# Kernel optimization log

Measured on AMD Instinct MI355X. Metric: run time of the kernel, lower is better.

Reference implementation:

```python
import jax, jax.numpy as jnp
import numpy as np

B, IMG_DIM, H, W = 2, 256, 64, 64
PC_C, PC_D = 16, 16          # voxel_dim = PC_C * PC_D = 256
VOXEL_DIM = PC_C * PC_D
QK_DIM = 256                 # out_channels of img_conv / voxel_conv


def _conv1x1(x, w, b):
    # x: [B, Cin, H, W], w: [Cout, Cin], b: [Cout]  (1x1 conv == per-pixel matmul)
    return jnp.einsum('bchw,oc->bohw', x, w) + b[None, :, None, None]


def setup_inputs() -> dict:
    key = jax.random.key(0)
    ks = jax.random.split(key, 10)
    s = 0.02
    return {
        'img': jax.random.normal(ks[0], (B, IMG_DIM, H, W), jnp.float32),
        'pc': jax.random.normal(ks[1], (B, PC_D, H, W, PC_C), jnp.float32),  # dense() layout [B,D,H,W,C]
        'img_conv_w': jax.random.normal(ks[2], (QK_DIM, IMG_DIM), jnp.float32) * s,
        'img_conv_b': jnp.zeros((QK_DIM,), jnp.float32),
        'voxel_conv_w': jax.random.normal(ks[3], (QK_DIM, VOXEL_DIM), jnp.float32) * s,
        'voxel_conv_b': jnp.zeros((QK_DIM,), jnp.float32),
        'img_v_w': jax.random.normal(ks[4], (IMG_DIM, IMG_DIM), jnp.float32) * s,
        'img_v_b': jnp.zeros((IMG_DIM,), jnp.float32),
        'voxel_v_w': jax.random.normal(ks[5], (VOXEL_DIM, VOXEL_DIM), jnp.float32) * s,
        'voxel_v_b': jnp.zeros((VOXEL_DIM,), jnp.float32),
    }


def reference(img, pc, img_conv_w, img_conv_b, voxel_conv_w, voxel_conv_b,
              img_v_w, img_v_b, voxel_v_w, voxel_v_b):
    b, c_img, h, w = img.shape
    # pc.dense() -> permute(0,4,1,2,3) -> [B, C, D, H, W] -> [B, C*D, H, W]
    pc = jnp.transpose(pc, (0, 4, 1, 2, 3))
    pcb, pcc, pcd, pch, pcw = pc.shape
    pc2 = pc.reshape(pcb, pcc * pcd, pch, pcw)
    n = h * w  # == pch * pcw (required by the bmms)

    img_q = _conv1x1(img, img_conv_w, img_conv_b).reshape(b, QK_DIM, n).transpose(0, 2, 1)  # [B, N, 256]
    pc_k = _conv1x1(pc2, voxel_conv_w, voxel_conv_b).reshape(b, QK_DIM, n)                  # [B, 256, N]
    # unscaled single-head cross attention, softmax over voxel positions
    attn = jax.nn.softmax(jnp.einsum('bnc,bcm->bnm', img_q, pc_k), axis=-1)                 # [B, N_img, N_pc]

    img_v = _conv1x1(img, img_v_w, img_v_b).reshape(b, c_img, n)                            # [B, C_img, N]
    img_v = jnp.einsum('bcn,bmn->bcm', img_v, attn).reshape(b, c_img, h, w)                 # img_v @ attn^T

    pc_v = _conv1x1(pc2, voxel_v_w, voxel_v_b).reshape(b, pcc * pcd, n)                     # [B, C*D, N]
    pc_v = jnp.einsum('bcn,bmn->bcm', pc_v, attn).reshape(b, pcc, pcd, pch, pcw)
    return (img_v, pc_v)
```

## Files before the change

### kernel.cpp

```cpp
#include <hip/hip_runtime.h>
#include <hip/hip_bf16.h>


typedef __hip_bfloat16 bf16;
typedef __attribute__((ext_vector_type(8))) short bf16x8;
typedef __attribute__((ext_vector_type(4))) float f32x4;

#define AS1 __attribute__((address_space(1)))
#define AS3 __attribute__((address_space(3)))

__device__ __forceinline__ void gld_lds16(const bf16* g, bf16* s) {
    __builtin_amdgcn_global_load_lds((const AS1 void*)g, (AS3 void*)s, 16, 0, 0);
}

__device__ __forceinline__ bf16x8 cvt8(const float* __restrict__ p) {
    const float4 a = *(const float4*)p;
    const float4 b = *(const float4*)(p + 4);
    bf16 t[8];
    t[0] = __float2bfloat16(a.x); t[1] = __float2bfloat16(a.y);
    t[2] = __float2bfloat16(a.z); t[3] = __float2bfloat16(a.w);
    t[4] = __float2bfloat16(b.x); t[5] = __float2bfloat16(b.y);
    t[6] = __float2bfloat16(b.z); t[7] = __float2bfloat16(b.w);
    return *(const bf16x8*)t;
}

__global__ __launch_bounds__(256) void proj_kernel(
    const float* __restrict__ img, const float* __restrict__ pc,
    const float* __restrict__ Wq,  const float* __restrict__ bq,
    const float* __restrict__ Wk,  const float* __restrict__ bk,
    const float* __restrict__ Wvi, const float* __restrict__ bvi,
    const float* __restrict__ Wvp, const float* __restrict__ bvp,
    bf16* __restrict__ Qw, bf16* __restrict__ Ktw, bf16* __restrict__ Vall)
{
    __shared__ __align__(16) bf16 XT[64][264];

    const int blk = blockIdx.x;
    const int s   = blk >> 8;
    const int b   = (blk >> 7) & 1;
    const int g   = (blk >> 6) & 1;
    const int n0  = (blk & 63) * 64;
    const int tid = threadIdx.x;

    if (s == 0) {
        const float* src = img + b * 1048576;
        for (int k = 0; k < 16; k++) {
            const int i = tid + k * 256;
            const int cin = i >> 4, nl4 = (i & 15) * 4;
            const float4 v = *(const float4*)&src[cin * 4096 + n0 + nl4];
            XT[nl4 + 0][cin] = __float2bfloat16(v.x);
            XT[nl4 + 1][cin] = __float2bfloat16(v.y);
            XT[nl4 + 2][cin] = __float2bfloat16(v.z);
            XT[nl4 + 3][cin] = __float2bfloat16(v.w);
        }
    } else {
        const float* src = pc + b * 1048576;
        for (int k = 0; k < 16; k++) {
            const int d = k, u = tid;
            const int nl = u >> 2, c4 = (u & 3) * 4;
            const float4 v = *(const float4*)&src[d * 65536 + (n0 + nl) * 16 + c4];
            XT[nl][(c4 + 0) * 16 + d] = __float2bfloat16(v.x);
            XT[nl][(c4 + 1) * 16 + d] = __float2bfloat16(v.y);
            XT[nl][(c4 + 2) * 16 + d] = __float2bfloat16(v.z);
            XT[nl][(c4 + 3) * 16 + d] = __float2bfloat16(v.w);
        }
    }
    __syncthreads();

    const float* W = s ? (g ? Wvp : Wk) : (g ? Wvi : Wq);
    const float* Bv = s ? (g ? bvp : bk) : (g ? bvi : bq);

    const int wv = tid >> 6, lane = tid & 63, l16 = lane & 15, quad = lane >> 4;
    const int ob = wv * 64;

    f32x4 acc[4][4] = {};

    for (int ks = 0; ks < 8; ks++) {
        const int k0 = ks * 32;
        bf16x8 af[4], wf[4];
        for (int ti = 0; ti < 4; ti++)
            af[ti] = *(const bf16x8*)&XT[ti * 16 + l16][k0 + quad * 8];
        for (int tj = 0; tj < 4; tj++)
            wf[tj] = cvt8(&W[(ob + tj * 16 + l16) * 256 + k0 + quad * 8]);
        for (int ti = 0; ti < 4; ti++)
            for (int tj = 0; tj < 4; tj++)
                acc[ti][tj] = __builtin_amdgcn_mfma_f32_16x16x32_bf16(af[ti], wf[tj], acc[ti][tj], 0, 0, 0);
    }

    if (g == 0) {
        bf16* D1 = (s ? Ktw : Qw) + b * (4096 * 256);
        for (int tj = 0; tj < 4; tj++) {
            const int o = ob + tj * 16 + l16;
            const float bias = Bv[o];
            for (int ti = 0; ti < 4; ti++) {
                const int nl = ti * 16 + quad * 4;
                for (int r = 0; r < 4; r++)
                    D1[(n0 + nl + r) * 256 + o] = __float2bfloat16(acc[ti][tj][r] + bias);
            }
        }
    } else {
        bf16* D2 = Vall + b * (512 * 4096) + (s ? 256 * 4096 : 0);
        for (int tj = 0; tj < 4; tj++) {
            const int o = ob + tj * 16 + l16;
            const float bias = Bv[o];
            for (int ti = 0; ti < 4; ti++) {
                const int nl = ti * 16 + quad * 4;
                bf16 pv[4];
                for (int r = 0; r < 4; r++)
                    pv[r] = __float2bfloat16(acc[ti][tj][r] + bias);
                *(uint2*)&D2[o * 4096 + n0 + nl] = *(const uint2*)pv;
            }
        }
    }
}

__global__ __launch_bounds__(256) void attn_s_kernel(
    const bf16* __restrict__ Qw, const bf16* __restrict__ Ktw,
    bf16* __restrict__ Pt, float* __restrict__ Lpart)
{
    __shared__ __align__(16) bf16 As[128 * 32];
    __shared__ __align__(16) bf16 Bs[128 * 32];

    const int b  = blockIdx.z;
    const int q0 = blockIdx.y * 128;
    const int p0 = blockIdx.x * 128;
    const bf16* A = Qw  + b * (4096 * 256);
    const bf16* B = Ktw + b * (4096 * 256);

    const int tid = threadIdx.x;
    const int wv = tid >> 6, lane = tid & 63, l16 = lane & 15, quad = lane >> 4;
    const int wr = wv >> 1, wc = wv & 1;

    f32x4 acc[4][4] = {};

    for (int ks = 0; ks < 8; ks++) {
        const int k0 = ks * 32;
        bf16x8 av[2], bv[2];
        for (int c = 0; c < 2; c++) {
            const int ci = c * 256 + tid;
            const int row = ci >> 2, kc = ci & 3;
            av[c] = *(const bf16x8*)&A[(q0 + row) * 256 + k0 + kc * 8];
            bv[c] = *(const bf16x8*)&B[(p0 + row) * 256 + k0 + kc * 8];
        }
        __syncthreads();
        for (int c = 0; c < 2; c++) {
            const int ci = c * 256 + tid;
            *(bf16x8*)&As[ci * 8] = av[c];
            *(bf16x8*)&Bs[ci * 8] = bv[c];
        }
        __syncthreads();
        bf16x8 af[4], bfr[4];
        for (int t = 0; t < 4; t++) {
            af[t]  = *(const bf16x8*)&As[(wr * 64 + t * 16 + l16) * 32 + quad * 8];
            bfr[t] = *(const bf16x8*)&Bs[(wc * 64 + t * 16 + l16) * 32 + quad * 8];
        }
        for (int ti = 0; ti < 4; ti++)
            for (int tj = 0; tj < 4; tj++)
                acc[ti][tj] = __builtin_amdgcn_mfma_f32_16x16x32_bf16(af[ti], bfr[tj], acc[ti][tj], 0, 0, 0);
    }

    bf16* Pdst = Pt + (size_t)b * 4096 * 4096;
    const int strip = blockIdx.x * 2 + wc;
    for (int ti = 0; ti < 4; ti++) {
        for (int r = 0; r < 4; r++) {
            const int qrow = wr * 64 + ti * 16 + quad * 4 + r;
            const int q = q0 + qrow;
            float partial = 0.0f;
            for (int tj = 0; tj < 4; tj++) {
                const float e = __expf(fminf(acc[ti][tj][r], 80.0f));
                partial += e;
                Pdst[(size_t)q * 4096 + p0 + wc * 64 + tj * 16 + l16] = __float2bfloat16(e);
            }
            partial += __shfl_xor(partial, 1);
            partial += __shfl_xor(partial, 2);
            partial += __shfl_xor(partial, 4);
            partial += __shfl_xor(partial, 8);
            if (l16 == 0)
                Lpart[(size_t)(b * 4096 + q) * 64 + strip] = partial;
        }
    }
}

__global__ __launch_bounds__(256) void lred_kernel(
    const float* __restrict__ Lpart, float* __restrict__ Linv)
{
    const int row = blockIdx.x * 256 + threadIdx.x;
    const float4* lp = (const float4*)&Lpart[(size_t)row * 64];
    float s = 0.0f;
    for (int i = 0; i < 16; i++) {
        const float4 v = lp[i];
        s += v.x + v.y + v.z + v.w;
    }
    Linv[row] = 1.0f / fmaxf(s, 1e-30f);
}

__global__ __launch_bounds__(256) void attn_o_kernel(
    const bf16* __restrict__ Vall, const bf16* __restrict__ Pt,
    const float* __restrict__ Linv, float* __restrict__ out)
{
    __shared__ __align__(16) bf16 As[128 * 32];
    __shared__ __align__(16) bf16 Bs[64 * 32];

    const int b  = blockIdx.z;
    const int c0 = blockIdx.y * 128;
    const int q0 = blockIdx.x * 64;
    const bf16* A = Vall + (size_t)b * 512 * 4096;
    const bf16* B = Pt   + (size_t)b * 4096 * 4096;

    const int tid = threadIdx.x;
    const int wv = tid >> 6, lane = tid & 63, l16 = lane & 15, quad = lane >> 4;
    const int wr = wv >> 1, wc = wv & 1;

    f32x4 acc[4][2] = {};

    const int arow = tid >> 2, akc = tid & 3;
    for (int ks = 0; ks < 128; ks++) {
        const int k0 = ks * 32;
        gld_lds16(A + (c0 + arow) * 4096 + k0 + akc * 8, As + tid * 8);
        gld_lds16(A + (c0 + 64 + arow) * 4096 + k0 + akc * 8, As + 2048 + tid * 8);
        gld_lds16(B + (q0 + arow) * 4096 + k0 + akc * 8, Bs + tid * 8);
        __syncthreads();
        bf16x8 af[4], bfr[2];
        for (int t = 0; t < 4; t++)
            af[t]  = *(const bf16x8*)&As[(wr * 64 + t * 16 + l16) * 32 + quad * 8];
        for (int t = 0; t < 2; t++)
            bfr[t] = *(const bf16x8*)&Bs[(wc * 32 + t * 16 + l16) * 32 + quad * 8];
        for (int ti = 0; ti < 4; ti++)
            for (int tj = 0; tj < 2; tj++)
                acc[ti][tj] = __builtin_amdgcn_mfma_f32_16x16x32_bf16(af[ti], bfr[tj], acc[ti][tj], 0, 0, 0);
        __syncthreads();
    }

    float rl[2];
    for (int tj = 0; tj < 2; tj++)
        rl[tj] = Linv[b * 4096 + q0 + wc * 32 + tj * 16 + l16];

    for (int ti = 0; ti < 4; ti++) {
        for (int r = 0; r < 4; r++) {
            const int c_ = c0 + wr * 64 + ti * 16 + quad * 4 + r;
            const size_t base = (c_ < 256)
                ? ((size_t)b * 1048576 + (size_t)c_ * 4096)
                : (2097152u + (size_t)b * 1048576 + (size_t)(c_ - 256) * 4096);
            for (int tj = 0; tj < 2; tj++) {
                const int q = q0 + wc * 32 + tj * 16 + l16;
                out[base + q] = acc[ti][tj][r] * rl[tj];
            }
        }
    }
}

extern "C" void kernel_launch(void* const* d_in, const int* in_sizes, int n_in,
                              void* d_out, int out_size, void* d_ws, size_t ws_size,
                              hipStream_t stream)
{
    const float* img = (const float*)d_in[0];
    const float* pc  = (const float*)d_in[1];
    const float* Wq  = (const float*)d_in[2];
    const float* bq  = (const float*)d_in[3];
    const float* Wk  = (const float*)d_in[4];
    const float* bk  = (const float*)d_in[5];
    const float* Wvi = (const float*)d_in[6];
    const float* bvi = (const float*)d_in[7];
    const float* Wvp = (const float*)d_in[8];
    const float* bvp = (const float*)d_in[9];

    char* ws = (char*)d_ws;
    bf16*  Qw    = (bf16*)(ws);
    bf16*  Ktw   = (bf16*)(ws + (4ull  << 20));
    bf16*  Vall  = (bf16*)(ws + (8ull  << 20));
    bf16*  Pt    = (bf16*)(ws + (16ull << 20));
    float* Lpart = (float*)(ws + (80ull << 20));
    float* Linv  = (float*)(ws + (82ull << 20));

    proj_kernel<<<512, 256, 0, stream>>>(img, pc, Wq, bq, Wk, bk,
                                         Wvi, bvi, Wvp, bvp, Qw, Ktw, Vall);
    attn_s_kernel<<<dim3(32, 32, 2), 256, 0, stream>>>(Qw, Ktw, Pt, Lpart);
    lred_kernel<<<32, 256, 0, stream>>>(Lpart, Linv);
    attn_o_kernel<<<dim3(64, 4, 2), 256, 0, stream>>>(Vall, Pt, Linv, (float*)d_out);
}
```

Baseline: 211.6 us.

## Split attn_o K-loop across four wave groups with LDS reduction and swizzle

The attn_o GEMM now runs with 1024 threads per block. Four 256-thread groups each handle a quarter of the K dimension, and their partial accumulators are then reduced through shared memory. An XOR swizzle is applied to the LDS layout to cut bank conflicts, and the epilogue writes vectorized float4 stores with a per-column Linv scale. The goal is more waves in flight to hide memory latency, since the old grid had only 512 blocks of 4 waves. The cost is a serialized LDS reduction and higher per-block register and LDS use.

```diff
diff --git a/kernel.cpp b/kernel.cpp
--- a/kernel.cpp
+++ b/kernel.cpp
@@ -193,12 +193,11 @@
     Linv[row] = 1.0f / fmaxf(s, 1e-30f);
 }
 
-__global__ __launch_bounds__(256) void attn_o_kernel(
+__global__ __launch_bounds__(1024, 8) void attn_o_kernel(
     const bf16* __restrict__ Vall, const bf16* __restrict__ Pt,
     const float* __restrict__ Linv, float* __restrict__ out)
 {
-    __shared__ __align__(16) bf16 As[128 * 32];
-    __shared__ __align__(16) bf16 Bs[64 * 32];
+    __shared__ __align__(16) bf16 smem[4][6144];
 
     const int b  = blockIdx.z;
     const int c0 = blockIdx.y * 128;
@@ -207,45 +206,78 @@
     const bf16* B = Pt   + (size_t)b * 4096 * 4096;
 
     const int tid = threadIdx.x;
-    const int wv = tid >> 6, lane = tid & 63, l16 = lane & 15, quad = lane >> 4;
+    const int grp = tid >> 8;
+    const int t8  = tid & 255;
+    const int wv = t8 >> 6, lane = t8 & 63, l16 = lane & 15, quad = lane >> 4;
     const int wr = wv >> 1, wc = wv & 1;
 
+    bf16* As = smem[grp];
+    bf16* Bs = smem[grp] + 4096;
+
+    int aoff[4], boff[2];
+    for (int t = 0; t < 4; t++) {
+        const int row = wr * 64 + t * 16 + l16;
+        aoff[t] = row * 32 + (quad ^ ((row >> 1) & 3)) * 8;
+    }
+    for (int t = 0; t < 2; t++) {
+        const int row = wc * 32 + t * 16 + l16;
+        boff[t] = row * 32 + (quad ^ ((row >> 1) & 3)) * 8;
+    }
+
+    const int arow = t8 >> 2;
+    const int kswz = ((t8 & 3) ^ ((arow >> 1) & 3)) * 8;
+
     f32x4 acc[4][2] = {};
 
-    const int arow = tid >> 2, akc = tid & 3;
-    for (int ks = 0; ks < 128; ks++) {
-        const int k0 = ks * 32;
-        gld_lds16(A + (c0 + arow) * 4096 + k0 + akc * 8, As + tid * 8);
-        gld_lds16(A + (c0 + 64 + arow) * 4096 + k0 + akc * 8, As + 2048 + tid * 8);
-        gld_lds16(B + (q0 + arow) * 4096 + k0 + akc * 8, Bs + tid * 8);
+    for (int ks = 0; ks < 32; ks++) {
+        const int k0 = grp * 1024 + ks * 32 + kswz;
+        gld_lds16(A + (c0 + arow) * 4096 + k0, As + t8 * 8);
+        gld_lds16(A + (c0 + 64 + arow) * 4096 + k0, As + 2048 + t8 * 8);
+        gld_lds16(B + (q0 + arow) * 4096 + k0, Bs + t8 * 8);
         __syncthreads();
         bf16x8 af[4], bfr[2];
-        for (int t = 0; t < 4; t++)
-            af[t]  = *(const bf16x8*)&As[(wr * 64 + t * 16 + l16) * 32 + quad * 8];
-        for (int t = 0; t < 2; t++)
-            bfr[t] = *(const bf16x8*)&Bs[(wc * 32 + t * 16 + l16) * 32 + quad * 8];
+        for (int t = 0; t < 4; t++) af[t]  = *(const bf16x8*)&As[aoff[t]];
+        for (int t = 0; t < 2; t++) bfr[t] = *(const bf16x8*)&Bs[boff[t]];
         for (int ti = 0; ti < 4; ti++)
             for (int tj = 0; tj < 2; tj++)
                 acc[ti][tj] = __builtin_amdgcn_mfma_f32_16x16x32_bf16(af[ti], bfr[tj], acc[ti][tj], 0, 0, 0);
         __syncthreads();
     }
 
-    float rl[2];
-    for (int tj = 0; tj < 2; tj++)
-        rl[tj] = Linv[b * 4096 + q0 + wc * 32 + tj * 16 + l16];
-
-    for (int ti = 0; ti < 4; ti++) {
-        for (int r = 0; r < 4; r++) {
-            const int c_ = c0 + wr * 64 + ti * 16 + quad * 4 + r;
-            const size_t base = (c_ < 256)
-                ? ((size_t)b * 1048576 + (size_t)c_ * 4096)
-                : (2097152u + (size_t)b * 1048576 + (size_t)(c_ - 256) * 4096);
-            for (int tj = 0; tj < 2; tj++) {
-                const int q = q0 + wc * 32 + tj * 16 + l16;
-                out[base + q] = acc[ti][tj][r] * rl[tj];
-            }
-        }
-    }
+    float* comb = (float*)&smem[0][0];
+    const int sl0 = (wr * 64 + quad * 4) * 64 + wc * 32 + l16;
+    if (grp == 0) {
+        for (int ti = 0; ti < 4; ti++)
+            for (int tj = 0; tj < 2; tj++)
+                for (int r = 0; r < 4; r++)
+                    comb[sl0 + (ti * 16 + r) * 64 + tj * 16] = acc[ti][tj][r];
+    }
+    __syncthreads();
+    for (int g = 1; g < 4; g++) {
+        if (grp == g) {
+            for (int ti = 0; ti < 4; ti++)
+                for (int tj = 0; tj < 2; tj++)
+                    for (int r = 0; r < 4; r++)
+                        comb[sl0 + (ti * 16 + r) * 64 + tj * 16] += acc[ti][tj][r];
+        }
+        __syncthreads();
+    }
+
+    const int f0 = tid * 8;
+    const int cl = f0 >> 6, ql = f0 & 63;
+    const int c_ = c0 + cl;
+    const size_t base = (c_ < 256)
+        ? ((size_t)b * 1048576 + (size_t)c_ * 4096)
+        : (2097152u + (size_t)b * 1048576 + (size_t)(c_ - 256) * 4096);
+    const float4 v0 = *(const float4*)&comb[f0];
+    const float4 v1 = *(const float4*)&comb[f0 + 4];
+    const float4 l0 = *(const float4*)&Linv[b * 4096 + q0 + ql];
+    const float4 l1 = *(const float4*)&Linv[b * 4096 + q0 + ql + 4];
+    float4 o0, o1;
+    o0.x = v0.x * l0.x; o0.y = v0.y * l0.y; o0.z = v0.z * l0.z; o0.w = v0.w * l0.w;
+    o1.x = v1.x * l1.x; o1.y = v1.y * l1.y; o1.z = v1.z * l1.z; o1.w = v1.w * l1.w;
+    *(float4*)&out[base + q0 + ql]     = o0;
+    *(float4*)&out[base + q0 + ql + 4] = o1;
 }
 
 extern "C" void kernel_launch(void* const* d_in, const int* in_sizes, int n_in,
@@ -275,5 +307,5 @@
                                          Wvi, bvi, Wvp, bvp, Qw, Ktw, Vall);
     attn_s_kernel<<<dim3(32, 32, 2), 256, 0, stream>>>(Qw, Ktw, Pt, Lpart);
     lred_kernel<<<32, 256, 0, stream>>>(Lpart, Linv);
-    attn_o_kernel<<<dim3(64, 4, 2), 256, 0, stream>>>(Vall, Pt, Linv, (float*)d_out);
-}
+    attn_o_kernel<<<dim3(64, 4, 2), 1024, 0, stream>>>(Vall, Pt, Linv, (float*)d_out);
+}
```

Result: faster. 202.7 us (-4.2%).

## Restructure attention output GEMM with larger tiles, split-K atomics and double-buffered LDS

Applied to the files above, without the earlier changes.

The attn_o kernel now uses 512-thread blocks with 256x128 output tiles, so the large P matrix is streamed half as many times. K is split four ways, and partial results are combined with relaxed float atomics into an output buffer that is zeroed first by a memset. The main loop double-buffers global-to-LDS loads, uses an XOR swizzle against LDS bank conflicts, and raises wave priority around the MFMAs. Blocks are remapped to group related tiles per XCD. The cost is extra atomic write traffic and a memset, and the summation order is no longer deterministic.

```diff
diff --git a/kernel.cpp b/kernel.cpp
--- a/kernel.cpp
+++ b/kernel.cpp
@@ -193,16 +193,23 @@
     Linv[row] = 1.0f / fmaxf(s, 1e-30f);
 }
 
-__global__ __launch_bounds__(256) void attn_o_kernel(
+__global__ __launch_bounds__(512, 4) void attn_o_kernel(
     const bf16* __restrict__ Vall, const bf16* __restrict__ Pt,
     const float* __restrict__ Linv, float* __restrict__ out)
 {
-    __shared__ __align__(16) bf16 As[128 * 32];
-    __shared__ __align__(16) bf16 Bs[64 * 32];
-
-    const int b  = blockIdx.z;
-    const int c0 = blockIdx.y * 128;
-    const int q0 = blockIdx.x * 64;
+    __shared__ __align__(16) bf16 smem[2][12288];
+
+    const int orig = blockIdx.x;
+    const int L = (orig & 7) * 64 + (orig >> 3);
+    const int c  = L & 1;
+    const int q  = (L >> 1) & 31;
+    const int kspl = (L >> 6) & 3;
+    const int b  = L >> 8;
+
+    const int c0 = c * 256;
+    const int q0 = q * 128;
+    const int kbase = kspl * 1024;
+
     const bf16* A = Vall + (size_t)b * 512 * 4096;
     const bf16* B = Pt   + (size_t)b * 4096 * 4096;
 
@@ -210,40 +217,73 @@
     const int wv = tid >> 6, lane = tid & 63, l16 = lane & 15, quad = lane >> 4;
     const int wr = wv >> 1, wc = wv & 1;
 
-    f32x4 acc[4][2] = {};
-
-    const int arow = tid >> 2, akc = tid & 3;
-    for (int ks = 0; ks < 128; ks++) {
-        const int k0 = ks * 32;
-        gld_lds16(A + (c0 + arow) * 4096 + k0 + akc * 8, As + tid * 8);
-        gld_lds16(A + (c0 + 64 + arow) * 4096 + k0 + akc * 8, As + 2048 + tid * 8);
-        gld_lds16(B + (q0 + arow) * 4096 + k0 + akc * 8, Bs + tid * 8);
-        __syncthreads();
-        bf16x8 af[4], bfr[2];
-        for (int t = 0; t < 4; t++)
-            af[t]  = *(const bf16x8*)&As[(wr * 64 + t * 16 + l16) * 32 + quad * 8];
-        for (int t = 0; t < 2; t++)
-            bfr[t] = *(const bf16x8*)&Bs[(wc * 32 + t * 16 + l16) * 32 + quad * 8];
+    int aoff[4], boff[4];
+    for (int t = 0; t < 4; t++) {
+        const int rowa = wr * 64 + t * 16 + l16;
+        aoff[t] = rowa * 32 + (quad ^ ((rowa >> 1) & 3)) * 8;
+        const int rowb = wc * 64 + t * 16 + l16;
+        boff[t] = rowb * 32 + (quad ^ ((rowb >> 1) & 3)) * 8;
+    }
+
+    const int arow = tid >> 2;
+    const int kswz = ((tid & 3) ^ ((arow >> 1) & 3)) * 8;
+    const bf16* Ag0 = A + (c0 + arow) * 4096 + kbase + kswz;
+    const bf16* Ag1 = A + (c0 + 128 + arow) * 4096 + kbase + kswz;
+    const bf16* Bg  = B + (size_t)(q0 + arow) * 4096 + kbase + kswz;
+
+    f32x4 acc[4][4] = {};
+
+#define STAGE(buf, ks)                                                  \
+    do {                                                                \
+        const int _k = (ks) * 32;                                       \
+        bf16* _s = &smem[(buf)][0];                                     \
+        gld_lds16(Ag0 + _k, _s + tid * 8);                              \
+        gld_lds16(Ag1 + _k, _s + 4096 + tid * 8);                       \
+        gld_lds16(Bg  + _k, _s + 8192 + tid * 8);                       \
+    } while (0)
+
+    STAGE(0, 0);
+    int cur = 0;
+    for (int ks = 0; ks < 32; ks++) {
+        if (ks + 1 < 32) {
+            STAGE(cur ^ 1, ks + 1);
+            asm volatile("s_waitcnt vmcnt(3)" ::: "memory");
+        } else {
+            asm volatile("s_waitcnt vmcnt(0)" ::: "memory");
+        }
+        __builtin_amdgcn_s_barrier();
+        __builtin_amdgcn_sched_barrier(0);
+
+        const bf16* As_ = &smem[cur][0];
+        const bf16* Bs_ = &smem[cur][8192];
+        bf16x8 af[4], bfr[4];
+        for (int t = 0; t < 4; t++) af[t]  = *(const bf16x8*)&As_[aoff[t]];
+        for (int t = 0; t < 4; t++) bfr[t] = *(const bf16x8*)&Bs_[boff[t]];
+        __builtin_amdgcn_s_setprio(1);
         for (int ti = 0; ti < 4; ti++)
-            for (int tj = 0; tj < 2; tj++)
+            for (int tj = 0; tj < 4; tj++)
                 acc[ti][tj] = __builtin_amdgcn_mfma_f32_16x16x32_bf16(af[ti], bfr[tj], acc[ti][tj], 0, 0, 0);
-        __syncthreads();
-    }
-
-    float rl[2];
-    for (int tj = 0; tj < 2; tj++)
-        rl[tj] = Linv[b * 4096 + q0 + wc * 32 + tj * 16 + l16];
-
+        __builtin_amdgcn_s_setprio(0);
+
+        asm volatile("s_waitcnt lgkmcnt(0)" ::: "memory");
+        __builtin_amdgcn_s_barrier();
+        cur ^= 1;
+    }
+#undef STAGE
+
+    float linv[4];
+    for (int tj = 0; tj < 4; tj++)
+        linv[tj] = Linv[b * 4096 + q0 + wc * 64 + tj * 16 + l16];
+
+    float* outp = out + (c0 ? 2097152u : 0u) + (size_t)b * 1048576;
     for (int ti = 0; ti < 4; ti++) {
         for (int r = 0; r < 4; r++) {
-            const int c_ = c0 + wr * 64 + ti * 16 + quad * 4 + r;
-            const size_t base = (c_ < 256)
-                ? ((size_t)b * 1048576 + (size_t)c_ * 4096)
-                : (2097152u + (size_t)b * 1048576 + (size_t)(c_ - 256) * 4096);
-            for (int tj = 0; tj < 2; tj++) {
-                const int q = q0 + wc * 32 + tj * 16 + l16;
-                out[base + q] = acc[ti][tj][r] * rl[tj];
-            }
+            const int crow = wr * 64 + ti * 16 + quad * 4 + r;
+            float* rowp = outp + (size_t)crow * 4096 + q0 + wc * 64;
+            for (int tj = 0; tj < 4; tj++)
+                __hip_atomic_fetch_add(&rowp[tj * 16 + l16],
+                                       acc[ti][tj][r] * linv[tj],
+                                       __ATOMIC_RELAXED, __HIP_MEMORY_SCOPE_AGENT);
         }
     }
 }
@@ -271,9 +311,10 @@
     float* Lpart = (float*)(ws + (80ull << 20));
     float* Linv  = (float*)(ws + (82ull << 20));
 
+    hipMemsetAsync(d_out, 0, (size_t)out_size, stream);
     proj_kernel<<<512, 256, 0, stream>>>(img, pc, Wq, bq, Wk, bk,
                                          Wvi, bvi, Wvp, bvp, Qw, Ktw, Vall);
     attn_s_kernel<<<dim3(32, 32, 2), 256, 0, stream>>>(Qw, Ktw, Pt, Lpart);
     lred_kernel<<<32, 256, 0, stream>>>(Lpart, Linv);
-    attn_o_kernel<<<dim3(64, 4, 2), 256, 0, stream>>>(Vall, Pt, Linv, (float*)d_out);
-}
+    attn_o_kernel<<<512, 512, 0, stream>>>(Vall, Pt, Linv, (float*)d_out);
+}
```

New measurement: 245.9 us. +16.2%, slower.
